# Kernel optimization log

Hardware: AMD Instinct MI355X
Metric: run time of the kernel (lower is better)

The kernel has to match this reference:

```python
import jax, jax.numpy as jnp
import numpy as np

LS, BS, N_HID, N_ENS = 1, 32, 256, 64
SEQ, D_IN, M_OBS = 64, 256, 64


def setup_inputs() -> dict:
    key = jax.random.key(0)
    ks = jax.random.split(key, 10)
    s = 1.0 / np.sqrt(N_HID)
    return {
        "x": jax.random.normal(ks[0], (BS, SEQ, D_IN), jnp.float32),
        "y": jax.random.normal(ks[1], (BS, M_OBS), jnp.float32),
        "enkf_state": jax.random.normal(ks[2], (LS, BS, N_HID, N_ENS), jnp.float32),
        "W_ih": jax.random.normal(ks[3], (D_IN, 4 * N_HID), jnp.float32) * s,
        "W_hh": jax.random.normal(ks[4], (N_HID, 4 * N_HID), jnp.float32) * s,
        "b": jnp.zeros((4 * N_HID,), jnp.float32),
        "Wh": jax.random.normal(ks[5], (M_OBS, N_HID), jnp.float32) * s,
        "bh": jnp.zeros((M_OBS,), jnp.float32),
        "q": jnp.asarray(1.0, jnp.float32),
        "e": jnp.asarray(0.1, jnp.float32),
        "r": jnp.asarray(0.5, jnp.float32),
        "eps_h": jax.random.normal(ks[6], (N_ENS // 2, LS, BS, N_HID), jnp.float32),
        "eps_c": jax.random.normal(ks[7], (N_ENS // 2, LS, BS, N_HID), jnp.float32),
        "train": 1,
    }


def reference(x, y, enkf_state, W_ih, W_hh, b, Wh, bh, q, e, r, eps_h, eps_c, train):
    ls, bs, n, N = enkf_state.shape
    mid = N // 2
    nq = jnp.sqrt(q * q)  # noise std = sqrt(q^2), keeps q differentiable in graph
    ne = jnp.sqrt(e * e)

    # ---- forecast: LSTM transition per ensemble member (vmapped, ls == 1) ----
    xs = jnp.swapaxes(x, 0, 1)  # [seq, bs, d_in]

    def lstm_member(h0, c0, eh, ec):  # h0,c0: [ls,bs,n]
        def step(carry, xt):
            h, c = carry
            g = xt @ W_ih + h @ W_hh + b  # [bs, 4n]
            i, f, gg, o = jnp.split(g, 4, axis=-1)
            c2 = jax.nn.sigmoid(f) * c + jax.nn.sigmoid(i) * jnp.tanh(gg)
            h2 = jax.nn.sigmoid(o) * jnp.tanh(c2)
            return (h2, c2), None
        (hT, cT), _ = jax.lax.scan(step, (h0[0], c0[0]), xs)
        return (hT + nq * eh[0])[None], (cT + ne * ec[0])[None]

    h0s = jnp.moveaxis(enkf_state[..., :mid], -1, 0)  # [mid, ls, bs, n]
    c0s = jnp.moveaxis(enkf_state[..., mid:], -1, 0)
    hN, cN = jax.vmap(lstm_member)(h0s, c0s, eps_h, eps_c)
    state = jnp.moveaxis(jnp.concatenate([hN, cN], axis=0), 0, -1)  # [ls,bs,n,N]

    eye_m = jnp.eye(M_OBS, dtype=state.dtype)

    def obs(s):  # observation model on last LSTM layer: [bs, m, N]
        return jnp.einsum('mn,bnN->bmN', Wh, s[-1]) + bh[:, None]

    def estimate(hxi):
        mu = hxi.mean(-1)  # [bs, m]
        cd = hxi - mu[..., None]
        cov = cd @ jnp.swapaxes(cd, -1, -2) / (N - 1) + eye_m * (r * r)
        return mu, cov

    def enkf_update(s):
        hxi = obs(s)
        hx, P = estimate(hxi)
        HA = hxi - hx[..., None]               # [bs, m, N]
        A = s - s.mean(-1)[..., None]          # [ls, bs, n, N]
        innov = y[:, :, None] - hxi            # [bs, m, N]
        sol = jnp.linalg.solve(P, innov)       # inv(P) @ innov
        G = jnp.einsum('lbnN,bmN->lbnm', A, HA)
        return s + jnp.einsum('lbnm,bmN->lbnN', G, sol) / (N - 1)

    def loglik_nis(mu, sig):
        S = sig + 1e-6 * eye_m
        L = jnp.linalg.cholesky(S)
        innov = y - mu
        v = jax.scipy.linalg.cho_solve((L, True), innov[..., None])[..., 0]
        quad = jnp.sum(innov * v, axis=-1)  # innov^T S^{-1} innov per batch
        logdet = 2.0 * jnp.sum(jnp.log(jnp.diagonal(L, axis1=-2, axis2=-1)), axis=-1)
        l = jnp.sum(-0.5 * logdet - 0.5 * quad)
        nis = jnp.mean(quad)
        return l, nis

    if train:  # training branch: filter first, then estimate on filtered ensemble
        state = enkf_update(state)
        mu, sig = estimate(obs(state))
        l, nis = loglik_nis(mu, sig)
        return mu, sig, state, l, nis
    else:      # eval branch: estimate on forecast, then filter
        mu, sig = estimate(obs(state))
        l, nis = loglik_nis(mu, sig)
        state = enkf_update(state)
        return mu, sig, state, l, nis
```

## Files before the change

kernel.cpp:

```cpp
#include <hip/hip_runtime.h>
#include <hip/hip_bf16.h>


typedef _Float16 f16;
typedef _Float16 f16x8 __attribute__((ext_vector_type(8)));
typedef _Float16 h4 __attribute__((ext_vector_type(4)));
typedef float f32x4 __attribute__((ext_vector_type(4)));

#define BS   32
#define NH   256
#define NE   64
#define SEQQ 64
#define DIN  256
#define MOBS 64
#define G4   1024

__device__ __forceinline__ float fast_sigmoid(float x) {
  return __builtin_amdgcn_rcpf(1.f + __expf(-x));
}
__device__ __forceinline__ float fast_tanh(float x) {
  return 2.f * __builtin_amdgcn_rcpf(1.f + __expf(-2.f * x)) - 1.f;
}

__device__ __forceinline__ void ldl_factor8(float* Pm, int tid) {
  const int lane = tid & 63, wave = tid >> 6;
  for (int kb = 0; kb < 64; kb += 8) {
    if (wave == 0) {
      float rl[8];
#pragma unroll
      for (int d = 0; d < 8; ++d) rl[d] = Pm[lane * 65 + kb + d];
#pragma unroll
      for (int kk = 0; kk < 8; ++kk) {
        float dk = __shfl(rl[kk], kb + kk);
        float fm = rl[kk] * __builtin_amdgcn_rcpf(dk);
#pragma unroll
        for (int jj = kk + 1; jj < 8; ++jj) {
          float cj = __shfl(rl[kk], kb + jj);
          if (lane > kb + kk) rl[jj] -= fm * cj;
        }
      }
#pragma unroll
      for (int d = 0; d < 8; ++d)
        if (lane >= kb) Pm[lane * 65 + kb + d] = rl[d];
    }
    __syncthreads();
    if (kb < 56) {
      const int n = lane;
      if (n >= kb + 8) {
        float ln[8];
#pragma unroll
        for (int d = 0; d < 8; ++d)
          ln[d] = Pm[n * 65 + kb + d] *
                  __builtin_amdgcn_rcpf(Pm[(kb + d) * 65 + kb + d]);
        for (int m = kb + 8 + wave; m < 64; m += 4) {
          float s = Pm[m * 65 + n];
#pragma unroll
          for (int d = 0; d < 8; ++d) s -= Pm[m * 65 + kb + d] * ln[d];
          Pm[m * 65 + n] = s;
        }
      }
      __syncthreads();
    }
  }
}

__global__ __launch_bounds__(256)
void k_pack(const float* __restrict__ W_hh, const float* __restrict__ W_ih,
            const float* __restrict__ Wh, f16* __restrict__ Wpack,
            f16* __restrict__ WpackIh, f16* __restrict__ WhfP,
            float* __restrict__ l_out, float* __restrict__ nis_out) {
  const int blk = blockIdx.x, tid = threadIdx.x;
  if (blk < 32) {
    const float* src = (blk & 1) ? W_ih : W_hh;
    f16* dst = (blk & 1) ? WpackIh : Wpack;
    const int kh = blk >> 1;
    __shared__ f16 ls[16][1032];
    for (int idx = tid; idx < 16 * 1024; idx += 256) {
      int kr = idx >> 10, n2 = idx & 1023;
      ls[kr][n2] = (f16)src[(size_t)(kh * 16 + kr) * G4 + n2];
    }
    __syncthreads();
    const int ks = kh >> 1;
    const int lane = tid & 63;
    const int qd = lane >> 4, c0 = lane & 15;
    if ((qd >> 1) == (kh & 1)) {
      const int krow = (qd & 1) * 8;
      for (int tile = tid >> 6; tile < 64; tile += 4) {
        f16x8 v;
#pragma unroll
        for (int j = 0; j < 8; ++j) v[j] = ls[krow + j][tile * 16 + c0];
        *(f16x8*)&dst[(size_t)((tile * 8 + ks) * 64 + lane) * 8] = v;
      }
    }
  } else {
    if (tid == 0) { l_out[0] = 0.f; nis_out[0] = 0.f; }
    for (int g = tid; g < 2048; g += 256) {
      int lane = g & 63, ks = (g >> 6) & 7, mt = g >> 9;
      int row = mt * 16 + (lane & 15);
      int k0 = ks * 32 + (lane >> 4) * 8;
#pragma unroll
      for (int j = 0; j < 8; ++j)
        WhfP[g * 8 + j] = (f16)Wh[row * NH + k0 + j];
    }
  }
}

__global__ __launch_bounds__(512, 2)
void k_xw(const float* __restrict__ x, const f16* __restrict__ WpackIh,
          const float* __restrict__ bv, h4* __restrict__ xwH) {
  __shared__ __align__(16) f16 xs[16 * 264];
  const int tid = threadIdx.x;
  const int m0 = blockIdx.x * 16;
  const int b = m0 >> 6, t0 = m0 & 63;
  const int g4 = b >> 4, br = b & 15;
  const int lane = tid & 63, w = tid >> 6;
  const int c0 = lane & 15, qd = lane >> 4;
  const int w0 = w * 32;
  for (int idx = tid; idx < 16 * 256; idx += 512) {
    int r = idx >> 8, k = idx & 255;
    xs[r * 264 + k] = (f16)x[(size_t)(m0 + r) * 256 + k];
  }
  __syncthreads();
  f16x8 afr[8];
#pragma unroll
  for (int ks = 0; ks < 8; ++ks)
    afr[ks] = *(const f16x8*)&xs[c0 * 264 + ks * 32 + qd * 8];
  const f16* wp0 = WpackIh + (size_t)lane * 8;
  f32x4 acc[8];
#pragma unroll
  for (int tt = 0; tt < 8; ++tt) {
    const int tg = ((tt >> 1) << 4) + w * 2 + (tt & 1);
    const f16* p = wp0 + (size_t)tg * 4096;
    f16x8 bf[8];
#pragma unroll
    for (int ks = 0; ks < 8; ++ks) bf[ks] = *(const f16x8*)(p + ks * 512);
    f32x4 a0 = {0.f, 0.f, 0.f, 0.f}, a1 = {0.f, 0.f, 0.f, 0.f};
#pragma unroll
    for (int ks = 0; ks < 8; ks += 2) {
      a0 = __builtin_amdgcn_mfma_f32_16x16x32_f16(afr[ks], bf[ks], a0, 0, 0, 0);
      a1 = __builtin_amdgcn_mfma_f32_16x16x32_f16(afr[ks + 1], bf[ks + 1], a1, 0, 0, 0);
    }
    acc[tt] = a0 + a1;
  }
#pragma unroll
  for (int nt = 0; nt < 2; ++nt) {
    const int j = w0 + nt * 16 + c0;
#pragma unroll
    for (int q = 0; q < 4; ++q) {
      const int t = t0 + qd * 4 + q;
      h4 v;
      v[0] = (f16)(acc[0 + nt][q] + bv[j]);
      v[1] = (f16)(acc[2 + nt][q] + bv[256 + j]);
      v[2] = (f16)(acc[4 + nt][q] + bv[512 + j]);
      v[3] = (f16)(acc[6 + nt][q] + bv[768 + j]);
      xwH[((size_t)(g4 * 64 + t) * 16 + br) * 256 + j] = v;
    }
  }
}

template <bool LAST>
__device__ __forceinline__ void lstm_step(
    int t, const f16* hcur, f16* hnxt, const f16* wg0, const f16* wg1,
    const f16* gbase, const f16x8 (&wres)[8], int c0, int qd, int j, int b0,
    int e, const h4* xwbase, f16x8 (&bf)[2][2], float (&creg)[4],
    const float* __restrict__ eps_h, const float* __restrict__ eps_c,
    float nq, float nee, float* __restrict__ stateF2) {
  h4 xw[4];
#pragma unroll
  for (int q = 0; q < 4; ++q)
    xw[q] = xwbase[(size_t)(t * 16 + qd * 4 + q) * 256 + j];

  f32x4 acc0 = {0.f, 0.f, 0.f, 0.f}, acc1 = {0.f, 0.f, 0.f, 0.f};
  f32x4 acc2 = {0.f, 0.f, 0.f, 0.f}, acc3 = {0.f, 0.f, 0.f, 0.f};
#pragma unroll
  for (int ks = 0; ks < 8; ++ks) {
    f16x8 afr = *(const f16x8*)&hcur[c0 * 264 + ks * 32 + qd * 8];
    f16x8 gbf = *(const f16x8*)(gbase + ks * 512);
    const int k2 = (ks + 1) & 7;
    bf[(ks + 1) & 1][0] = *(const f16x8*)(wg0 + k2 * 512);
    bf[(ks + 1) & 1][1] = *(const f16x8*)(wg1 + k2 * 512);
    acc0 = __builtin_amdgcn_mfma_f32_16x16x32_f16(afr, bf[ks & 1][0], acc0, 0, 0, 0);
    acc1 = __builtin_amdgcn_mfma_f32_16x16x32_f16(afr, bf[ks & 1][1], acc1, 0, 0, 0);
    acc2 = __builtin_amdgcn_mfma_f32_16x16x32_f16(afr, gbf, acc2, 0, 0, 0);
    acc3 = __builtin_amdgcn_mfma_f32_16x16x32_f16(afr, wres[ks], acc3, 0, 0, 0);
  }

#pragma unroll
  for (int q = 0; q < 4; ++q) {
    const int r = qd * 4 + q;
    float iv = acc0[q] + (float)xw[q][0];
    float fv = acc1[q] + (float)xw[q][1];
    float gv = acc2[q] + (float)xw[q][2];
    float ov = acc3[q] + (float)xw[q][3];
    float c2 = fast_sigmoid(fv) * creg[q] + fast_sigmoid(iv) * fast_tanh(gv);
    float h2 = fast_sigmoid(ov) * fast_tanh(c2);
    creg[q] = c2;
    if (!LAST) {
      hnxt[r * 264 + j] = (f16)h2;
    } else {
      stateF2[((size_t)e * 32 + b0 + r) * 256 + j] =
          h2 + nq * eps_h[(e * BS + b0 + r) * NH + j];
      stateF2[((size_t)(32 + e) * 32 + b0 + r) * 256 + j] =
          c2 + nee * eps_c[(e * BS + b0 + r) * NH + j];
    }
  }
  if (!LAST) __syncthreads();
}

__global__ __launch_bounds__(1024)
void k_lstm(const h4* __restrict__ xwH, const f16* __restrict__ Wpack,
            const float* __restrict__ enkf, const float* __restrict__ eps_h,
            const float* __restrict__ eps_c, const float* __restrict__ qp,
            const float* __restrict__ ep, float* __restrict__ stateF2) {
  __shared__ __align__(16) f16 glds[65536];
  __shared__ __align__(16) f16 hs[2][16 * 264];
  const int tid = threadIdx.x;
  const int e = blockIdx.x >> 1;
  const int g4 = blockIdx.x & 1;
  const int b0 = g4 * 16;
  const int lane = tid & 63;
  const int ws = tid >> 6;
  const int c0 = lane & 15;
  const int qd = lane >> 4;
  const int j = ws * 16 + c0;

  {
    const f16* gsrc = Wpack + 32 * 4096;
    for (int i = tid; i < 8192; i += 1024)
      *(f16x8*)&glds[i * 8] = *(const f16x8*)&gsrc[(size_t)i * 8];
  }
  f16x8 wres[8];
  {
    const f16* op = Wpack + (size_t)(48 + ws) * 4096 + (size_t)lane * 8;
#pragma unroll
    for (int ks = 0; ks < 8; ++ks) wres[ks] = *(const f16x8*)(op + ks * 512);
  }
  for (int idx = tid; idx < 16 * 256; idx += 1024) {
    int r = idx >> 8, nh = idx & 255;
    hs[0][r * 264 + nh] = (f16)enkf[((b0 + r) * NH + nh) * NE + e];
  }
  float creg[4];
#pragma unroll
  for (int q = 0; q < 4; ++q)
    creg[q] = enkf[((b0 + qd * 4 + q) * NH + j) * NE + 32 + e];

  const float nq = fabsf(qp[0]);
  const float nee = fabsf(ep[0]);

  const f16* wg0 = Wpack + (size_t)(0 * 16 + ws) * 4096 + (size_t)lane * 8;
  const f16* wg1 = Wpack + (size_t)(1 * 16 + ws) * 4096 + (size_t)lane * 8;
  const f16* gbase = glds + (size_t)ws * 4096 + (size_t)lane * 8;

  f16x8 bf[2][2];
  bf[0][0] = *(const f16x8*)(wg0);
  bf[0][1] = *(const f16x8*)(wg1);

  const h4* xwbase = xwH + (size_t)g4 * 64 * 16 * 256;
  __syncthreads();

  for (int t = 0; t < 62; t += 2) {
    lstm_step<false>(t, hs[0], hs[1], wg0, wg1, gbase, wres, c0, qd, j, b0, e,
                     xwbase, bf, creg, eps_h, eps_c, nq, nee, stateF2);
    lstm_step<false>(t + 1, hs[1], hs[0], wg0, wg1, gbase, wres, c0, qd, j, b0,
                     e, xwbase, bf, creg, eps_h, eps_c, nq, nee, stateF2);
  }
  lstm_step<false>(62, hs[0], hs[1], wg0, wg1, gbase, wres, c0, qd, j, b0, e,
                   xwbase, bf, creg, eps_h, eps_c, nq, nee, stateF2);
  lstm_step<true>(63, hs[1], hs[0], wg0, wg1, gbase, wres, c0, qd, j, b0, e,
                  xwbase, bf, creg, eps_h, eps_c, nq, nee, stateF2);
}

__global__ __launch_bounds__(256)
void k_fused(const float* __restrict__ stateF2, const f16* __restrict__ WhfP,
             const float* __restrict__ bh, const float* __restrict__ rp,
             const float* __restrict__ y, float* __restrict__ mu_out,
             float* __restrict__ sig_out, float* __restrict__ state_out,
             float* __restrict__ l_out, float* __restrict__ nis_out) {
  __shared__ __align__(16) f16 stT[64 * 264];
  __shared__ float hxl[64 * 66];
  __shared__ float Pm[64 * 65];
  __shared__ __align__(16) f16 TT[64 * 72];
  __shared__ __align__(16) char U[36864];
  __shared__ float hxm[64];
  __shared__ float dinv[64];
  __shared__ float srm[256];

  const int tid = threadIdx.x, b = blockIdx.x;
  const int lane = tid & 63, wave = tid >> 6;
  const int c0 = lane & 15, qd = lane >> 4;
  const int n = tid & 63, mg = tid >> 6;
  const float r2 = rp[0] * rp[0];

  f16x8 whfr[8];
#pragma unroll
  for (int ks = 0; ks < 8; ++ks)
    whfr[ks] = *(const f16x8*)&WhfP[(((size_t)wave * 8 + ks) * 64 + lane) * 8];

  for (int idx = tid; idx < NH * NE; idx += 256) {
    int j = idx >> 8, k = idx & 255;
    stT[j * 264 + k] = (f16)stateF2[((size_t)j * 32 + b) * 256 + k];
  }
  __syncthreads();
  for (int nt = 0; nt < 4; ++nt) {
    f32x4 acc = {0.f, 0.f, 0.f, 0.f};
#pragma unroll
    for (int ks = 0; ks < 8; ++ks) {
      f16x8 bfr = *(const f16x8*)&stT[(nt * 16 + c0) * 264 + ks * 32 + qd * 8];
      acc = __builtin_amdgcn_mfma_f32_16x16x32_f16(whfr[ks], bfr, acc, 0, 0, 0);
    }
#pragma unroll
    for (int q = 0; q < 4; ++q)
      hxl[(wave * 16 + qd * 4 + q) * 66 + nt * 16 + c0] = acc[q] + bh[wave * 16 + qd * 4 + q];
  }
  __syncthreads();
  if (tid < 64) {
    float s = 0.f;
    for (int j = 0; j < 64; ++j) s += hxl[tid * 66 + j];
    hxm[tid] = s * (1.f / 64.f);
  }
  __syncthreads();
  {
    f16* HAf = (f16*)U;
    for (int idx = tid; idx < 4096; idx += 256) {
      int m = idx >> 6, j = idx & 63;
      HAf[m * 72 + j] = (f16)(hxl[m * 66 + j] - hxm[m]);
    }
    __syncthreads();
    f16x8 afr[2];
#pragma unroll
    for (int ks = 0; ks < 2; ++ks)
      afr[ks] = *(const f16x8*)&HAf[(wave * 16 + c0) * 72 + ks * 32 + qd * 8];
    for (int nt = 0; nt < 4; ++nt) {
      f32x4 acc = {0.f, 0.f, 0.f, 0.f};
#pragma unroll
      for (int ks = 0; ks < 2; ++ks) {
        f16x8 bfr = *(const f16x8*)&HAf[(nt * 16 + c0) * 72 + ks * 32 + qd * 8];
        acc = __builtin_amdgcn_mfma_f32_16x16x32_f16(afr[ks], bfr, acc, 0, 0, 0);
      }
#pragma unroll
      for (int q = 0; q < 4; ++q) {
        int m1 = wave * 16 + qd * 4 + q, m2 = nt * 16 + c0;
        Pm[m1 * 65 + m2] = acc[q] * (1.f / 63.f) + (m1 == m2 ? r2 : 0.f);
      }
    }
  }
  __syncthreads();

  {
    float* R = (float*)U;
    f16* HAT = (f16*)(U + 16384);
    f16* solT = (f16*)(U + 25600);
    for (int idx = tid; idx < 4096; idx += 256) {
      int m = idx >> 6, j = idx & 63;
      float hv = hxl[m * 66 + j];
      R[idx] = y[b * 64 + m] - hv;
      HAT[j * 72 + m] = (f16)(hv - hxm[m]);
    }
    __syncthreads();
    ldl_factor8(Pm, tid);
    if (tid < 64) dinv[tid] = __builtin_amdgcn_rcpf(Pm[tid * 65 + tid]);
    __syncthreads();
    for (int i0 = 0; i0 < 64; i0 += 8) {
      if (wave == 0) {
        float rl[8];
#pragma unroll
        for (int d = 0; d < 8; ++d) rl[d] = R[(i0 + d) * 64 + n];
#pragma unroll
        for (int a = 1; a < 8; ++a)
#pragma unroll
          for (int bq = 0; bq < a; ++bq)
            rl[a] -= Pm[(i0 + a) * 65 + i0 + bq] * dinv[i0 + bq] * rl[bq];
#pragma unroll
        for (int d = 1; d < 8; ++d) R[(i0 + d) * 64 + n] = rl[d];
      }
      __syncthreads();
      for (int m = i0 + 8 + mg; m < 64; m += 4) {
        float s = R[m * 64 + n];
#pragma unroll
        for (int d = 0; d < 8; ++d)
          s -= Pm[m * 65 + i0 + d] * dinv[i0 + d] * R[(i0 + d) * 64 + n];
        R[m * 64 + n] = s;
      }
      __syncthreads();
    }
    for (int idx = tid; idx < 4096; idx += 256) R[idx] *= dinv[idx >> 6];
    __syncthreads();
    for (int i0 = 56; i0 >= 0; i0 -= 8) {
      if (wave == 0) {
        float rl[8];
#pragma unroll
        for (int d = 0; d < 8; ++d) rl[d] = R[(i0 + d) * 64 + n];
#pragma unroll
        for (int a = 6; a >= 0; --a)
#pragma unroll
          for (int bq = 7; bq > a; --bq)
            rl[a] -= Pm[(i0 + bq) * 65 + i0 + a] * dinv[i0 + a] * rl[bq];
#pragma unroll
        for (int d = 0; d < 7; ++d) R[(i0 + d) * 64 + n] = rl[d];
      }
      __syncthreads();
      for (int m = mg; m < i0; m += 4) {
        float s = R[m * 64 + n];
        float dm = dinv[m];
#pragma unroll
        for (int d = 0; d < 8; ++d)
          s -= Pm[(i0 + d) * 65 + m] * dm * R[(i0 + d) * 64 + n];
        R[m * 64 + n] = s;
      }
      __syncthreads();
    }
    for (int idx = tid; idx < 4096; idx += 256) {
      int m = idx >> 6, j = idx & 63;
      solT[j * 72 + m] = (f16)R[m * 64 + j];
    }
    __syncthreads();
    f16x8 afr[2];
#pragma unroll
    for (int ks = 0; ks < 2; ++ks)
      afr[ks] = *(const f16x8*)&HAT[(wave * 16 + c0) * 72 + ks * 32 + qd * 8];
    for (int nt = 0; nt < 4; ++nt) {
      f32x4 acc = {0.f, 0.f, 0.f, 0.f};
#pragma unroll
      for (int ks = 0; ks < 2; ++ks) {
        f16x8 bfr = *(const f16x8*)&solT[(nt * 16 + c0) * 72 + ks * 32 + qd * 8];
        acc = __builtin_amdgcn_mfma_f32_16x16x32_f16(afr[ks], bfr, acc, 0, 0, 0);
      }
#pragma unroll
      for (int q = 0; q < 4; ++q) {
        int jp = wave * 16 + qd * 4 + q, j = nt * 16 + c0;
        TT[j * 72 + jp] = (f16)(acc[q] * (1.f / 63.f));
      }
    }
  }
  __syncthreads();

  {
    f16* Af = (f16*)U;
    for (int idx = tid; idx < NH * NE; idx += 256) {
      int j = idx >> 8, k = idx & 255;
      Af[k * 72 + j] = (f16)stateF2[((size_t)j * 32 + b) * 256 + k];
    }
    __syncthreads();
    {
      float s = 0.f;
      for (int j = 0; j < 64; ++j) s += (float)Af[tid * 72 + j];
      srm[tid] = s * (1.f / 64.f);
    }
    __syncthreads();
    for (int idx = tid; idx < NH * NE; idx += 256) {
      int nh = idx >> 6, j = idx & 63;
      Af[nh * 72 + j] = (f16)((float)Af[nh * 72 + j] - srm[nh]);
    }
    __syncthreads();
    f16x8 bfr[4][2];
#pragma unroll
    for (int nt = 0; nt < 4; ++nt)
#pragma unroll
      for (int ks = 0; ks < 2; ++ks)
        bfr[nt][ks] = *(const f16x8*)&TT[(nt * 16 + c0) * 72 + ks * 32 + qd * 8];
    for (int mt0 = 0; mt0 < 4; ++mt0) {
      int mt = wave * 4 + mt0;
      f16x8 afr[2];
#pragma unroll
      for (int ks = 0; ks < 2; ++ks)
        afr[ks] = *(const f16x8*)&Af[(mt * 16 + c0) * 72 + ks * 32 + qd * 8];
#pragma unroll
      for (int nt = 0; nt < 4; ++nt) {
        f32x4 acc = {0.f, 0.f, 0.f, 0.f};
#pragma unroll
        for (int ks = 0; ks < 2; ++ks)
          acc = __builtin_amdgcn_mfma_f32_16x16x32_f16(afr[ks], bfr[nt][ks], acc, 0, 0, 0);
#pragma unroll
        for (int q = 0; q < 4; ++q) {
          int m = mt * 16 + qd * 4 + q, j = nt * 16 + c0;
          float v = (float)Af[m * 72 + j] + srm[m] + acc[q];
          state_out[b * (NH * NE) + m * 64 + j] = v;
          stT[j * 264 + m] = (f16)v;
        }
      }
    }
  }
  __syncthreads();

  for (int nt = 0; nt < 4; ++nt) {
    f32x4 acc = {0.f, 0.f, 0.f, 0.f};
#pragma unroll
    for (int ks = 0; ks < 8; ++ks) {
      f16x8 bfr = *(const f16x8*)&stT[(nt * 16 + c0) * 264 + ks * 32 + qd * 8];
      acc = __builtin_amdgcn_mfma_f32_16x16x32_f16(whfr[ks], bfr, acc, 0, 0, 0);
    }
#pragma unroll
    for (int q = 0; q < 4; ++q)
      hxl[(wave * 16 + qd * 4 + q) * 66 + nt * 16 + c0] = acc[q] + bh[wave * 16 + qd * 4 + q];
  }
  __syncthreads();
  if (tid < 64) {
    float s = 0.f;
    for (int j = 0; j < 64; ++j) s += hxl[tid * 66 + j];
    s *= (1.f / 64.f);
    hxm[tid] = s;
    mu_out[b * MOBS + tid] = s;
  }
  __syncthreads();
  {
    f16* HAf = (f16*)U;
    for (int idx = tid; idx < 4096; idx += 256) {
      int m = idx >> 6, j = idx & 63;
      HAf[m * 72 + j] = (f16)(hxl[m * 66 + j] - hxm[m]);
    }
    __syncthreads();
    f16x8 afr[2];
#pragma unroll
    for (int ks = 0; ks < 2; ++ks)
      afr[ks] = *(const f16x8*)&HAf[(wave * 16 + c0) * 72 + ks * 32 + qd * 8];
    for (int nt = 0; nt < 4; ++nt) {
      f32x4 acc = {0.f, 0.f, 0.f, 0.f};
#pragma unroll
      for (int ks = 0; ks < 2; ++ks) {
        f16x8 bfr = *(const f16x8*)&HAf[(nt * 16 + c0) * 72 + ks * 32 + qd * 8];
        acc = __builtin_amdgcn_mfma_f32_16x16x32_f16(afr[ks], bfr, acc, 0, 0, 0);
      }
#pragma unroll
      for (int q = 0; q < 4; ++q) {
        int m1 = wave * 16 + qd * 4 + q, m2 = nt * 16 + c0;
        float v = acc[q] * (1.f / 63.f) + (m1 == m2 ? r2 : 0.f);
        sig_out[b * (MOBS * MOBS) + m1 * MOBS + m2] = v;
        Pm[m1 * 65 + m2] = v + (m1 == m2 ? 1e-6f : 0.f);
      }
    }
  }
  __syncthreads();

  ldl_factor8(Pm, tid);
  if (tid < 64) dinv[tid] = __builtin_amdgcn_rcpf(Pm[tid * 65 + tid]);
  __syncthreads();
  if (wave == 0) {
    const int m = lane;
    float rm = y[b * 64 + m] - hxm[m];
    const float r0 = rm;
    for (int i = 0; i < 63; ++i) {
      float xi = __shfl(rm, i);
      if (m > i) rm -= Pm[m * 65 + i] * dinv[i] * xi;
    }
    rm *= dinv[m];
    for (int i = 63; i >= 1; --i) {
      float xi = __shfl(rm, i);
      if (m < i) rm -= Pm[i * 65 + m] * dinv[m] * xi;
    }
    float prod = r0 * rm;
    float ld = __logf(Pm[m * 65 + m]);
#pragma unroll
    for (int off = 32; off; off >>= 1) {
      prod += __shfl_down(prod, off);
      ld += __shfl_down(ld, off);
    }
    if (m == 0) {
      atomicAdd(l_out, -0.5f * (ld + prod));
      atomicAdd(nis_out, prod * (1.f / 32.f));
    }
  }
}

extern "C" void kernel_launch(void* const* d_in, const int* in_sizes, int n_in,
                              void* d_out, int out_size, void* d_ws, size_t ws_size,
                              hipStream_t stream) {
  (void)in_sizes; (void)n_in; (void)out_size; (void)ws_size;
  const float* x     = (const float*)d_in[0];
  const float* y     = (const float*)d_in[1];
  const float* enkf  = (const float*)d_in[2];
  const float* W_ih  = (const float*)d_in[3];
  const float* W_hh  = (const float*)d_in[4];
  const float* bvec  = (const float*)d_in[5];
  const float* Wh    = (const float*)d_in[6];
  const float* bh    = (const float*)d_in[7];
  const float* qp    = (const float*)d_in[8];
  const float* ep    = (const float*)d_in[9];
  const float* rp    = (const float*)d_in[10];
  const float* eps_h = (const float*)d_in[11];
  const float* eps_c = (const float*)d_in[12];

  char* ws = (char*)d_ws;
  h4*    xwH     = (h4*)(ws);
  f16*   Wpack   = (f16*)(ws + 4194304);
  f16*   WpackIh = (f16*)(ws + 4718592);
  f16*   WhfP    = (f16*)(ws + 5242880);
  float* stateF2 = (float*)(ws + 5275648);

  float* out = (float*)d_out;
  float* mu_out    = out;
  float* sig_out   = out + 2048;
  float* state_out = out + 133120;
  float* l_out     = out + 657408;
  float* nis_out   = out + 657409;

  k_pack<<<33, 256, 0, stream>>>(W_hh, W_ih, Wh, Wpack, WpackIh, WhfP,
                                 l_out, nis_out);
  k_xw<<<128, 512, 0, stream>>>(x, WpackIh, bvec, xwH);
  k_lstm<<<64, 1024, 0, stream>>>(xwH, Wpack, enkf, eps_h, eps_c, qp, ep, stateF2);
  k_fused<<<32, 256, 0, stream>>>(stateF2, WhfP, bh, rp, y, mu_out, sig_out,
                                  state_out, l_out, nis_out);
}
```

Measured before the change: 416.1 us.

## Keep i/f/o recurrent weights in registers as FP8, converting to FP16 per step

The pack kernel now also writes an FP8 copy of W_hh. The LSTM kernel holds the input, forget and output gate weight fragments in registers as packed FP8 and expands them to FP16 before each MFMA. Previously two of those gates streamed from global memory on every timestep and only the output gate stayed in registers. This removes per-step global weight loads from the serial recurrence, at the cost of extra conversion instructions and reduced weight precision, which can hurt accuracy over 64 steps.

```diff
diff --git a/kernel.cpp b/kernel.cpp
--- a/kernel.cpp
+++ b/kernel.cpp
@@ -6,6 +6,8 @@
 typedef _Float16 f16x8 __attribute__((ext_vector_type(8)));
 typedef _Float16 h4 __attribute__((ext_vector_type(4)));
 typedef float f32x4 __attribute__((ext_vector_type(4)));
+typedef float f32x2v __attribute__((ext_vector_type(2)));
+typedef int i32x2 __attribute__((ext_vector_type(2)));
 
 #define BS   32
 #define NH   256
@@ -22,6 +24,17 @@
   return 2.f * __builtin_amdgcn_rcpf(1.f + __expf(-2.f * x)) - 1.f;
 }
 
+__device__ __forceinline__ f16x8 cvt8(i32x2 v) {
+  f32x2v a0 = __builtin_amdgcn_cvt_pk_f32_fp8(v.x, false);
+  f32x2v a1 = __builtin_amdgcn_cvt_pk_f32_fp8(v.x, true);
+  f32x2v a2 = __builtin_amdgcn_cvt_pk_f32_fp8(v.y, false);
+  f32x2v a3 = __builtin_amdgcn_cvt_pk_f32_fp8(v.y, true);
+  f16x8 r;
+  r[0] = (f16)a0.x; r[1] = (f16)a0.y; r[2] = (f16)a1.x; r[3] = (f16)a1.y;
+  r[4] = (f16)a2.x; r[5] = (f16)a2.y; r[6] = (f16)a3.x; r[7] = (f16)a3.y;
+  return r;
+}
+
 __device__ __forceinline__ void ldl_factor8(float* Pm, int tid) {
   const int lane = tid & 63, wave = tid >> 6;
   for (int kb = 0; kb < 64; kb += 8) {
@@ -68,6 +81,7 @@
 void k_pack(const float* __restrict__ W_hh, const float* __restrict__ W_ih,
             const float* __restrict__ Wh, f16* __restrict__ Wpack,
             f16* __restrict__ WpackIh, f16* __restrict__ WhfP,
+            char* __restrict__ Wp8,
             float* __restrict__ l_out, float* __restrict__ nis_out) {
   const int blk = blockIdx.x, tid = threadIdx.x;
   if (blk < 32) {
@@ -90,6 +104,15 @@
 #pragma unroll
         for (int j = 0; j < 8; ++j) v[j] = ls[krow + j][tile * 16 + c0];
         *(f16x8*)&dst[(size_t)((tile * 8 + ks) * 64 + lane) * 8] = v;
+        if (!(blk & 1)) {
+          int lo = 0, hi = 0;
+          lo = __builtin_amdgcn_cvt_pk_fp8_f32((float)v[0], (float)v[1], lo, false);
+          lo = __builtin_amdgcn_cvt_pk_fp8_f32((float)v[2], (float)v[3], lo, true);
+          hi = __builtin_amdgcn_cvt_pk_fp8_f32((float)v[4], (float)v[5], hi, false);
+          hi = __builtin_amdgcn_cvt_pk_fp8_f32((float)v[6], (float)v[7], hi, true);
+          i32x2 w; w.x = lo; w.y = hi;
+          *(i32x2*)&Wp8[(size_t)((tile * 8 + ks) * 64 + lane) * 8] = w;
+        }
       }
     }
   } else {
@@ -160,9 +183,9 @@
 
 template <bool LAST>
 __device__ __forceinline__ void lstm_step(
-    int t, const f16* hcur, f16* hnxt, const f16* wg0, const f16* wg1,
-    const f16* gbase, const f16x8 (&wres)[8], int c0, int qd, int j, int b0,
-    int e, const h4* xwbase, f16x8 (&bf)[2][2], float (&creg)[4],
+    int t, const f16* hcur, f16* hnxt, const f16* gbase,
+    const i32x2 (&w8)[3][8], int c0, int qd, int j, int b0, int e,
+    const h4* xwbase, float (&creg)[4],
     const float* __restrict__ eps_h, const float* __restrict__ eps_c,
     float nq, float nee, float* __restrict__ stateF2) {
   h4 xw[4];
@@ -176,13 +199,13 @@
   for (int ks = 0; ks < 8; ++ks) {
     f16x8 afr = *(const f16x8*)&hcur[c0 * 264 + ks * 32 + qd * 8];
     f16x8 gbf = *(const f16x8*)(gbase + ks * 512);
-    const int k2 = (ks + 1) & 7;
-    bf[(ks + 1) & 1][0] = *(const f16x8*)(wg0 + k2 * 512);
-    bf[(ks + 1) & 1][1] = *(const f16x8*)(wg1 + k2 * 512);
-    acc0 = __builtin_amdgcn_mfma_f32_16x16x32_f16(afr, bf[ks & 1][0], acc0, 0, 0, 0);
-    acc1 = __builtin_amdgcn_mfma_f32_16x16x32_f16(afr, bf[ks & 1][1], acc1, 0, 0, 0);
+    f16x8 iw = cvt8(w8[0][ks]);
+    f16x8 fw = cvt8(w8[1][ks]);
+    f16x8 ow = cvt8(w8[2][ks]);
+    acc0 = __builtin_amdgcn_mfma_f32_16x16x32_f16(afr, iw, acc0, 0, 0, 0);
+    acc1 = __builtin_amdgcn_mfma_f32_16x16x32_f16(afr, fw, acc1, 0, 0, 0);
     acc2 = __builtin_amdgcn_mfma_f32_16x16x32_f16(afr, gbf, acc2, 0, 0, 0);
-    acc3 = __builtin_amdgcn_mfma_f32_16x16x32_f16(afr, wres[ks], acc3, 0, 0, 0);
+    acc3 = __builtin_amdgcn_mfma_f32_16x16x32_f16(afr, ow, acc3, 0, 0, 0);
   }
 
 #pragma unroll
@@ -209,9 +232,10 @@
 
 __global__ __launch_bounds__(1024)
 void k_lstm(const h4* __restrict__ xwH, const f16* __restrict__ Wpack,
-            const float* __restrict__ enkf, const float* __restrict__ eps_h,
-            const float* __restrict__ eps_c, const float* __restrict__ qp,
-            const float* __restrict__ ep, float* __restrict__ stateF2) {
+            const char* __restrict__ Wp8, const float* __restrict__ enkf,
+            const float* __restrict__ eps_h, const float* __restrict__ eps_c,
+            const float* __restrict__ qp, const float* __restrict__ ep,
+            float* __restrict__ stateF2) {
   __shared__ __align__(16) f16 glds[65536];
   __shared__ __align__(16) f16 hs[2][16 * 264];
   const int tid = threadIdx.x;
@@ -229,11 +253,16 @@
     for (int i = tid; i < 8192; i += 1024)
       *(f16x8*)&glds[i * 8] = *(const f16x8*)&gsrc[(size_t)i * 8];
   }
-  f16x8 wres[8];
+  i32x2 w8[3][8];
   {
-    const f16* op = Wpack + (size_t)(48 + ws) * 4096 + (size_t)lane * 8;
-#pragma unroll
-    for (int ks = 0; ks < 8; ++ks) wres[ks] = *(const f16x8*)(op + ks * 512);
+    const int tg[3] = {ws, 16 + ws, 48 + ws};
+#pragma unroll
+    for (int g = 0; g < 3; ++g) {
+      const char* p = Wp8 + (size_t)(tg[g] * 8) * 512 + (size_t)lane * 8;
+#pragma unroll
+      for (int ks = 0; ks < 8; ++ks)
+        w8[g][ks] = *(const i32x2*)(p + (size_t)ks * 512);
+    }
   }
   for (int idx = tid; idx < 16 * 256; idx += 1024) {
     int r = idx >> 8, nh = idx & 255;
@@ -246,28 +275,20 @@
 
   const float nq = fabsf(qp[0]);
   const float nee = fabsf(ep[0]);
-
-  const f16* wg0 = Wpack + (size_t)(0 * 16 + ws) * 4096 + (size_t)lane * 8;
-  const f16* wg1 = Wpack + (size_t)(1 * 16 + ws) * 4096 + (size_t)lane * 8;
   const f16* gbase = glds + (size_t)ws * 4096 + (size_t)lane * 8;
-
-  f16x8 bf[2][2];
-  bf[0][0] = *(const f16x8*)(wg0);
-  bf[0][1] = *(const f16x8*)(wg1);
-
   const h4* xwbase = xwH + (size_t)g4 * 64 * 16 * 256;
   __syncthreads();
 
   for (int t = 0; t < 62; t += 2) {
-    lstm_step<false>(t, hs[0], hs[1], wg0, wg1, gbase, wres, c0, qd, j, b0, e,
-                     xwbase, bf, creg, eps_h, eps_c, nq, nee, stateF2);
-    lstm_step<false>(t + 1, hs[1], hs[0], wg0, wg1, gbase, wres, c0, qd, j, b0,
-                     e, xwbase, bf, creg, eps_h, eps_c, nq, nee, stateF2);
-  }
-  lstm_step<false>(62, hs[0], hs[1], wg0, wg1, gbase, wres, c0, qd, j, b0, e,
-                   xwbase, bf, creg, eps_h, eps_c, nq, nee, stateF2);
-  lstm_step<true>(63, hs[1], hs[0], wg0, wg1, gbase, wres, c0, qd, j, b0, e,
-                  xwbase, bf, creg, eps_h, eps_c, nq, nee, stateF2);
+    lstm_step<false>(t, hs[0], hs[1], gbase, w8, c0, qd, j, b0, e, xwbase,
+                     creg, eps_h, eps_c, nq, nee, stateF2);
+    lstm_step<false>(t + 1, hs[1], hs[0], gbase, w8, c0, qd, j, b0, e, xwbase,
+                     creg, eps_h, eps_c, nq, nee, stateF2);
+  }
+  lstm_step<false>(62, hs[0], hs[1], gbase, w8, c0, qd, j, b0, e, xwbase,
+                   creg, eps_h, eps_c, nq, nee, stateF2);
+  lstm_step<true>(63, hs[1], hs[0], gbase, w8, c0, qd, j, b0, e, xwbase,
+                  creg, eps_h, eps_c, nq, nee, stateF2);
 }
 
 __global__ __launch_bounds__(256)
@@ -585,6 +606,7 @@
   f16*   WpackIh = (f16*)(ws + 4718592);
   f16*   WhfP    = (f16*)(ws + 5242880);
   float* stateF2 = (float*)(ws + 5275648);
+  char*  Wp8     = (char*)(ws + 7372800);
 
   float* out = (float*)d_out;
   float* mu_out    = out;
@@ -593,10 +615,11 @@
   float* l_out     = out + 657408;
   float* nis_out   = out + 657409;
 
-  k_pack<<<33, 256, 0, stream>>>(W_hh, W_ih, Wh, Wpack, WpackIh, WhfP,
+  k_pack<<<33, 256, 0, stream>>>(W_hh, W_ih, Wh, Wpack, WpackIh, WhfP, Wp8,
                                  l_out, nis_out);
   k_xw<<<128, 512, 0, stream>>>(x, WpackIh, bvec, xwH);
-  k_lstm<<<64, 1024, 0, stream>>>(xwH, Wpack, enkf, eps_h, eps_c, qp, ep, stateF2);
+  k_lstm<<<64, 1024, 0, stream>>>(xwH, Wpack, Wp8, enkf, eps_h, eps_c, qp, ep,
+                                  stateF2);
   k_fused<<<32, 256, 0, stream>>>(stateF2, WhfP, bh, rp, y, mu_out, sig_out,
                                   state_out, l_out, nis_out);
 }
```

New measurement: 425.8 us. 2.3% more time.

## Split each LSTM recurrence across four cooperating blocks with global-memory h exchange

Applied to the files above, without the earlier changes.

The recurrent LSTM kernel moves from 64 blocks of 1024 threads to 256 blocks of 256 threads. Four blocks now share one (ensemble member, batch half) cluster, and each owns a quarter of the hidden units, with its W_hh slice held fully in LDS instead of partly in registers and global memory. After every timestep, each block publishes its slice of h to global memory and waits on an atomic counter barrier, then gathers the other three slices. This spreads work over more CUs and keeps all weights in LDS, at the cost of a cross-block spin barrier and global round trips on the serial 64-step critical path. It also relies on all 256 blocks being co-resident.

```diff
diff --git a/kernel.cpp b/kernel.cpp
--- a/kernel.cpp
+++ b/kernel.cpp
@@ -68,6 +68,7 @@
 void k_pack(const float* __restrict__ W_hh, const float* __restrict__ W_ih,
             const float* __restrict__ Wh, f16* __restrict__ Wpack,
             f16* __restrict__ WpackIh, f16* __restrict__ WhfP,
+            int* __restrict__ cnt,
             float* __restrict__ l_out, float* __restrict__ nis_out) {
   const int blk = blockIdx.x, tid = threadIdx.x;
   if (blk < 32) {
@@ -94,6 +95,7 @@
     }
   } else {
     if (tid == 0) { l_out[0] = 0.f; nis_out[0] = 0.f; }
+    if (tid < 64) cnt[tid] = 0;
     for (int g = tid; g < 2048; g += 256) {
       int lane = g & 63, ks = (g >> 6) & 7, mt = g >> 9;
       int row = mt * 16 + (lane & 15);
@@ -159,42 +161,38 @@
 }
 
 template <bool LAST>
-__device__ __forceinline__ void lstm_step(
-    int t, const f16* hcur, f16* hnxt, const f16* wg0, const f16* wg1,
-    const f16* gbase, const f16x8 (&wres)[8], int c0, int qd, int j, int b0,
-    int e, const h4* xwbase, f16x8 (&bf)[2][2], float (&creg)[4],
+__device__ __forceinline__ void lstm_step_cl(
+    int t, const f16* hcur, f16* hnxt, const f16* wb0, const f16* wb1,
+    const f16* wb2, const f16* wb3, int c0, int qd, int j, int b0, int e,
+    const h4* xwbase, float (&creg)[4],
     const float* __restrict__ eps_h, const float* __restrict__ eps_c,
     float nq, float nee, float* __restrict__ stateF2) {
   h4 xw[4];
 #pragma unroll
-  for (int q = 0; q < 4; ++q)
-    xw[q] = xwbase[(size_t)(t * 16 + qd * 4 + q) * 256 + j];
-
-  f32x4 acc0 = {0.f, 0.f, 0.f, 0.f}, acc1 = {0.f, 0.f, 0.f, 0.f};
-  f32x4 acc2 = {0.f, 0.f, 0.f, 0.f}, acc3 = {0.f, 0.f, 0.f, 0.f};
+  for (int qq = 0; qq < 4; ++qq)
+    xw[qq] = xwbase[(size_t)(t * 16 + qd * 4 + qq) * 256 + j];
+
+  f32x4 a0 = {0.f, 0.f, 0.f, 0.f}, a1 = {0.f, 0.f, 0.f, 0.f};
+  f32x4 a2 = {0.f, 0.f, 0.f, 0.f}, a3 = {0.f, 0.f, 0.f, 0.f};
 #pragma unroll
   for (int ks = 0; ks < 8; ++ks) {
     f16x8 afr = *(const f16x8*)&hcur[c0 * 264 + ks * 32 + qd * 8];
-    f16x8 gbf = *(const f16x8*)(gbase + ks * 512);
-    const int k2 = (ks + 1) & 7;
-    bf[(ks + 1) & 1][0] = *(const f16x8*)(wg0 + k2 * 512);
-    bf[(ks + 1) & 1][1] = *(const f16x8*)(wg1 + k2 * 512);
-    acc0 = __builtin_amdgcn_mfma_f32_16x16x32_f16(afr, bf[ks & 1][0], acc0, 0, 0, 0);
-    acc1 = __builtin_amdgcn_mfma_f32_16x16x32_f16(afr, bf[ks & 1][1], acc1, 0, 0, 0);
-    acc2 = __builtin_amdgcn_mfma_f32_16x16x32_f16(afr, gbf, acc2, 0, 0, 0);
-    acc3 = __builtin_amdgcn_mfma_f32_16x16x32_f16(afr, wres[ks], acc3, 0, 0, 0);
-  }
-
-#pragma unroll
-  for (int q = 0; q < 4; ++q) {
-    const int r = qd * 4 + q;
-    float iv = acc0[q] + (float)xw[q][0];
-    float fv = acc1[q] + (float)xw[q][1];
-    float gv = acc2[q] + (float)xw[q][2];
-    float ov = acc3[q] + (float)xw[q][3];
-    float c2 = fast_sigmoid(fv) * creg[q] + fast_sigmoid(iv) * fast_tanh(gv);
+    a0 = __builtin_amdgcn_mfma_f32_16x16x32_f16(afr, *(const f16x8*)(wb0 + ks * 512), a0, 0, 0, 0);
+    a1 = __builtin_amdgcn_mfma_f32_16x16x32_f16(afr, *(const f16x8*)(wb1 + ks * 512), a1, 0, 0, 0);
+    a2 = __builtin_amdgcn_mfma_f32_16x16x32_f16(afr, *(const f16x8*)(wb2 + ks * 512), a2, 0, 0, 0);
+    a3 = __builtin_amdgcn_mfma_f32_16x16x32_f16(afr, *(const f16x8*)(wb3 + ks * 512), a3, 0, 0, 0);
+  }
+
+#pragma unroll
+  for (int qq = 0; qq < 4; ++qq) {
+    const int r = qd * 4 + qq;
+    float iv = a0[qq] + (float)xw[qq][0];
+    float fv = a1[qq] + (float)xw[qq][1];
+    float gv = a2[qq] + (float)xw[qq][2];
+    float ov = a3[qq] + (float)xw[qq][3];
+    float c2 = fast_sigmoid(fv) * creg[qq] + fast_sigmoid(iv) * fast_tanh(gv);
     float h2 = fast_sigmoid(ov) * fast_tanh(c2);
-    creg[q] = c2;
+    creg[qq] = c2;
     if (!LAST) {
       hnxt[r * 264 + j] = (f16)h2;
     } else {
@@ -204,70 +202,91 @@
           c2 + nee * eps_c[(e * BS + b0 + r) * NH + j];
     }
   }
-  if (!LAST) __syncthreads();
-}
-
-__global__ __launch_bounds__(1024)
+}
+
+__global__ __launch_bounds__(256)
 void k_lstm(const h4* __restrict__ xwH, const f16* __restrict__ Wpack,
             const float* __restrict__ enkf, const float* __restrict__ eps_h,
             const float* __restrict__ eps_c, const float* __restrict__ qp,
-            const float* __restrict__ ep, float* __restrict__ stateF2) {
-  __shared__ __align__(16) f16 glds[65536];
+            const float* __restrict__ ep, float* __restrict__ stateF2,
+            f16* __restrict__ hXg, int* __restrict__ cnt) {
+  __shared__ __align__(16) f16 Wlds[65536];
   __shared__ __align__(16) f16 hs[2][16 * 264];
   const int tid = threadIdx.x;
-  const int e = blockIdx.x >> 1;
-  const int g4 = blockIdx.x & 1;
+  const int cl = blockIdx.x >> 2;
+  const int quad = blockIdx.x & 3;
+  const int e = cl >> 1;
+  const int g4 = cl & 1;
   const int b0 = g4 * 16;
   const int lane = tid & 63;
-  const int ws = tid >> 6;
+  const int w = tid >> 6;
   const int c0 = lane & 15;
   const int qd = lane >> 4;
-  const int j = ws * 16 + c0;
-
-  {
-    const f16* gsrc = Wpack + 32 * 4096;
-    for (int i = tid; i < 8192; i += 1024)
-      *(f16x8*)&glds[i * 8] = *(const f16x8*)&gsrc[(size_t)i * 8];
-  }
-  f16x8 wres[8];
-  {
-    const f16* op = Wpack + (size_t)(48 + ws) * 4096 + (size_t)lane * 8;
-#pragma unroll
-    for (int ks = 0; ks < 8; ++ks) wres[ks] = *(const f16x8*)(op + ks * 512);
-  }
-  for (int idx = tid; idx < 16 * 256; idx += 1024) {
+  const int jbase = quad * 64 + w * 16;
+  const int j = jbase + c0;
+
+  for (int ch = tid; ch < 8192; ch += 256) {
+    int tl = ch >> 9, off = ch & 511;
+    int tg = (tl >> 2) * 16 + quad * 4 + (tl & 3);
+    *(f16x8*)&Wlds[(size_t)ch * 8] = *(const f16x8*)&Wpack[((size_t)tg * 512 + off) * 8];
+  }
+  for (int idx = tid; idx < 4096; idx += 256) {
     int r = idx >> 8, nh = idx & 255;
     hs[0][r * 264 + nh] = (f16)enkf[((b0 + r) * NH + nh) * NE + e];
   }
   float creg[4];
 #pragma unroll
-  for (int q = 0; q < 4; ++q)
-    creg[q] = enkf[((b0 + qd * 4 + q) * NH + j) * NE + 32 + e];
+  for (int qq = 0; qq < 4; ++qq)
+    creg[qq] = enkf[((b0 + qd * 4 + qq) * NH + j) * NE + 32 + e];
 
   const float nq = fabsf(qp[0]);
   const float nee = fabsf(ep[0]);
-
-  const f16* wg0 = Wpack + (size_t)(0 * 16 + ws) * 4096 + (size_t)lane * 8;
-  const f16* wg1 = Wpack + (size_t)(1 * 16 + ws) * 4096 + (size_t)lane * 8;
-  const f16* gbase = glds + (size_t)ws * 4096 + (size_t)lane * 8;
-
-  f16x8 bf[2][2];
-  bf[0][0] = *(const f16x8*)(wg0);
-  bf[0][1] = *(const f16x8*)(wg1);
-
+  const f16* wb0 = Wlds + (size_t)(0 + w) * 4096 + (size_t)lane * 8;
+  const f16* wb1 = Wlds + (size_t)(4 + w) * 4096 + (size_t)lane * 8;
+  const f16* wb2 = Wlds + (size_t)(8 + w) * 4096 + (size_t)lane * 8;
+  const f16* wb3 = Wlds + (size_t)(12 + w) * 4096 + (size_t)lane * 8;
   const h4* xwbase = xwH + (size_t)g4 * 64 * 16 * 256;
   __syncthreads();
 
-  for (int t = 0; t < 62; t += 2) {
-    lstm_step<false>(t, hs[0], hs[1], wg0, wg1, gbase, wres, c0, qd, j, b0, e,
-                     xwbase, bf, creg, eps_h, eps_c, nq, nee, stateF2);
-    lstm_step<false>(t + 1, hs[1], hs[0], wg0, wg1, gbase, wres, c0, qd, j, b0,
-                     e, xwbase, bf, creg, eps_h, eps_c, nq, nee, stateF2);
-  }
-  lstm_step<false>(62, hs[0], hs[1], wg0, wg1, gbase, wres, c0, qd, j, b0, e,
-                   xwbase, bf, creg, eps_h, eps_c, nq, nee, stateF2);
-  lstm_step<true>(63, hs[1], hs[0], wg0, wg1, gbase, wres, c0, qd, j, b0, e,
-                  xwbase, bf, creg, eps_h, eps_c, nq, nee, stateF2);
+  for (int t = 0; t < 63; ++t) {
+    const int p = (t + 1) & 1;
+    lstm_step_cl<false>(t, hs[t & 1], hs[p], wb0, wb1, wb2, wb3, c0, qd, j,
+                        b0, e, xwbase, creg, eps_h, eps_c, nq, nee, stateF2);
+    __syncthreads();
+    {
+      const int r = lane >> 2, ch = (lane & 3) * 4;
+      unsigned long long v =
+          *(const unsigned long long*)&hs[p][r * 264 + jbase + ch];
+      __hip_atomic_store(
+          (unsigned long long*)&hXg[(((size_t)p * 64 + cl) * 16 + r) * 256 + jbase + ch],
+          v, __ATOMIC_RELAXED, __HIP_MEMORY_SCOPE_AGENT);
+    }
+    __syncthreads();
+    if (tid == 0) {
+      __hip_atomic_fetch_add(cnt + cl, 1, __ATOMIC_RELEASE,
+                             __HIP_MEMORY_SCOPE_AGENT);
+      const int target = 4 * (t + 1);
+      while (__hip_atomic_load(cnt + cl, __ATOMIC_ACQUIRE,
+                               __HIP_MEMORY_SCOPE_AGENT) < target)
+        __builtin_amdgcn_s_sleep(4);
+    }
+    __syncthreads();
+    {
+      const int r = tid >> 4, ch = (tid & 15) * 4;
+#pragma unroll
+      for (int s = 1; s < 4; ++s) {
+        const int q2 = (quad + s) & 3;
+        const int jj = q2 * 64 + ch;
+        unsigned long long v = __hip_atomic_load(
+            (const unsigned long long*)&hXg[(((size_t)p * 64 + cl) * 16 + r) * 256 + jj],
+            __ATOMIC_RELAXED, __HIP_MEMORY_SCOPE_AGENT);
+        *(unsigned long long*)&hs[p][r * 264 + jj] = v;
+      }
+    }
+    __syncthreads();
+  }
+  lstm_step_cl<true>(63, hs[1], hs[0], wb0, wb1, wb2, wb3, c0, qd, j, b0, e,
+                     xwbase, creg, eps_h, eps_c, nq, nee, stateF2);
 }
 
 __global__ __launch_bounds__(256)
@@ -585,6 +604,8 @@
   f16*   WpackIh = (f16*)(ws + 4718592);
   f16*   WhfP    = (f16*)(ws + 5242880);
   float* stateF2 = (float*)(ws + 5275648);
+  f16*   hXg     = (f16*)(ws + 7372800);
+  int*   cnt     = (int*)(ws + 8421376);
 
   float* out = (float*)d_out;
   float* mu_out    = out;
@@ -593,10 +614,11 @@
   float* l_out     = out + 657408;
   float* nis_out   = out + 657409;
 
-  k_pack<<<33, 256, 0, stream>>>(W_hh, W_ih, Wh, Wpack, WpackIh, WhfP,
+  k_pack<<<33, 256, 0, stream>>>(W_hh, W_ih, Wh, Wpack, WpackIh, WhfP, cnt,
                                  l_out, nis_out);
   k_xw<<<128, 512, 0, stream>>>(x, WpackIh, bvec, xwH);
-  k_lstm<<<64, 1024, 0, stream>>>(xwH, Wpack, enkf, eps_h, eps_c, qp, ep, stateF2);
+  k_lstm<<<256, 256, 0, stream>>>(xwH, Wpack, enkf, eps_h, eps_c, qp, ep,
+                                  stateF2, hXg, cnt);
   k_fused<<<32, 256, 0, stream>>>(stateF2, WhfP, bh, rp, y, mu_out, sig_out,
                                   state_out, l_out, nis_out);
 }
```

Result: slower. 918.2 us (+120.7%).
